# Kernel optimization log

Measured on AMD Instinct MI355X. Metric: run time of the kernel, lower is better.

The kernel has to match this reference:

```python
import jax, jax.numpy as jnp
import numpy as np

# Dims (match init_kwargs)
B, S, D = 2, 2048, 2048
H = 16
Q_LORA, KV_LORA = 768, 512
NOPE, ROPE, VD = 128, 64, 128
QHD = NOPE + ROPE  # 192


def setup_inputs() -> dict:
    key = jax.random.key(0)
    ks = jax.random.split(key, 7)
    w = lambda k, shape: (jax.random.normal(k, shape, jnp.float32) * 0.02)
    return {
        "x": jax.random.normal(ks[0], (B, S, D), jnp.float32),
        "position": jnp.broadcast_to(jnp.arange(S, dtype=jnp.int32), (B, S)),
        "mask": jnp.tril(jnp.ones((1, 1, S, S), jnp.int32)),  # causal
        "w_q_down": w(ks[1], (D, Q_LORA)),                 # (in, out) layout
        "w_q_up": w(ks[2], (Q_LORA, H * QHD)),
        "w_kv_down": w(ks[3], (D, KV_LORA + ROPE)),
        "w_kv_up": w(ks[4], (KV_LORA, H * (NOPE + VD))),
        "w_out": w(ks[5], (H * VD, D)),
    }


def reference(x, position, mask, w_q_down, w_q_up, w_kv_down, w_kv_up, w_out):
    # position unused: rope_embedding is None in the source module.
    # Low-rank Q: down then up projection.
    q = (x @ w_q_down) @ w_q_up                      # [B,S,H*QHD]
    q = q.reshape(B, S, H, QHD).transpose(0, 2, 1, 3)  # [B,H,S,QHD]
    q_nope, q_rope = q[..., :NOPE], q[..., NOPE:]

    # Low-rank KV: down projection yields compressed kv + shared rope key.
    c = x @ w_kv_down                                # [B,S,KV_LORA+ROPE]
    c_kv, k_rope = c[..., :KV_LORA], c[..., KV_LORA:]
    k_rope = k_rope[:, None, :, :]                   # [B,1,S,ROPE]

    kv = (c_kv @ w_kv_up).reshape(B, S, H, NOPE + VD).transpose(0, 2, 1, 3)
    k_nope, v = kv[..., :NOPE], kv[..., NOPE:]       # [B,H,S,NOPE], [B,H,S,VD]

    q_state = jnp.concatenate([q_nope, q_rope], axis=-1)           # [B,H,S,QHD]
    k_state = jnp.concatenate(
        [k_nope, jnp.broadcast_to(k_rope, (B, H, S, ROPE))], axis=-1)

    scale = 1.0 / jnp.sqrt(jnp.float32(VD))  # source divides by sqrt(v_head_dim)
    scores = jnp.einsum("bhqd,bhkd->bhqk", q_state, k_state) * scale
    scores = jnp.where(mask == 0, jnp.float32(-jnp.inf), scores)
    att = jax.nn.softmax(scores, axis=-1)            # dropout_rate=0 (eval)
    out = jnp.einsum("bhqk,bhkd->bhqd", att, v)      # [B,H,S,VD]
    out = out.transpose(0, 2, 1, 3).reshape(B, S, H * VD)
    return out @ w_out
```

## Files before the change

### kernel.cpp

```cpp
#include <hip/hip_runtime.h>

typedef __bf16 bf16;
typedef bf16 bf16x8 __attribute__((ext_vector_type(8)));
typedef bf16 bf16x4 __attribute__((ext_vector_type(4)));
typedef float f32x4 __attribute__((ext_vector_type(4)));
typedef short s16x4 __attribute__((ext_vector_type(4)));

#define AS1 __attribute__((address_space(1)))
#define AS3 __attribute__((address_space(3)))

__device__ __forceinline__ void load_lds16(const void* g, void* l) {
    __builtin_amdgcn_global_load_lds((const AS1 unsigned int*)g,
                                     (AS3 unsigned int*)l, 16, 0, 0);
}

__global__ __launch_bounds__(256) void cast_f32_bf16(
        const float* __restrict__ in, bf16* __restrict__ out, int n) {
    int i = (blockIdx.x * 256 + threadIdx.x) * 4;
    if (i < n) {
        float4 v = *(const float4*)(in + i);
        bf16x4 o = { (bf16)v.x, (bf16)v.y, (bf16)v.z, (bf16)v.w };
        *(bf16x4*)(out + i) = o;
    }
}

__global__ __launch_bounds__(256) void transpose_cast(
        const float* __restrict__ in, bf16* __restrict__ out,
        int K, int N, int Np) {
    __shared__ float tile[32][33];
    int bx = blockIdx.x * 32;
    int by = blockIdx.y * 32;
    int tx = threadIdx.x, ty = threadIdx.y;
#pragma unroll
    for (int i = 0; i < 4; ++i) {
        int k = by + ty + i * 8, n = bx + tx;
        float v = (k < K && n < N) ? in[(size_t)k * N + n] : 0.f;
        tile[ty + i * 8][tx] = v;
    }
    __syncthreads();
#pragma unroll
    for (int i = 0; i < 4; ++i) {
        int n = bx + ty + i * 8, k = by + tx;
        if (n < Np && k < K) out[(size_t)n * K + k] = (bf16)tile[tx][ty + i * 8];
    }
}

__global__ __launch_bounds__(256) void transpose_v(
        const bf16* __restrict__ kvb, bf16* __restrict__ vtb) {
    __shared__ bf16 t[32][34];
    const int kv0 = blockIdx.x * 32;
    const int vd0 = blockIdx.y * 32;
    const int bh = blockIdx.z;
    const int b = bh >> 4, h = bh & 15;
    const int tx = threadIdx.x, ty = threadIdx.y;
#pragma unroll
    for (int i = 0; i < 4; ++i)
        t[ty + i * 8][tx] = kvb[(size_t)(b * 2048 + kv0 + ty + i * 8) * 4096
                                + h * 256 + 128 + vd0 + tx];
    __syncthreads();
#pragma unroll
    for (int i = 0; i < 4; ++i)
        vtb[(size_t)(bh * 128 + vd0 + ty + i * 8) * 2048 + kv0 + tx] =
            t[tx][ty + i * 8];
}

template <typename OutT>
__global__ __launch_bounds__(256) void gemm_bt(
        const bf16* __restrict__ A, const bf16* __restrict__ Bt,
        OutT* __restrict__ C, int K, int lda, int ldb, int ldc) {
    __shared__ __align__(16) bf16 As[128 * 64];
    __shared__ __align__(16) bf16 Bs[128 * 64];
    const int tid = threadIdx.x;
    const int wave = tid >> 6, lane = tid & 63;
    const int l15 = lane & 15, quad = lane >> 4;
    const int m0 = blockIdx.y * 128, n0 = blockIdx.x * 128;
    const int wm = (wave >> 1) * 64, wn = (wave & 1) * 64;

    f32x4 acc[4][4] = {};

    for (int k0 = 0; k0 < K; k0 += 64) {
#pragma unroll
        for (int c = 0; c < 4; ++c) {
            int e = wave * 2048 + c * 512 + lane * 8;
            int r = e >> 6, col = e & 63;
            load_lds16(A + (size_t)(m0 + r) * lda + k0 + col,
                       &As[wave * 2048 + c * 512]);
            load_lds16(Bt + (size_t)(n0 + r) * ldb + k0 + col,
                       &Bs[wave * 2048 + c * 512]);
        }
        __syncthreads();
#pragma unroll
        for (int kk = 0; kk < 64; kk += 32) {
            bf16x8 af[4], bf[4];
#pragma unroll
            for (int i = 0; i < 4; ++i)
                af[i] = *(const bf16x8*)&As[(wm + i * 16 + l15) * 64 + kk + quad * 8];
#pragma unroll
            for (int j = 0; j < 4; ++j)
                bf[j] = *(const bf16x8*)&Bs[(wn + j * 16 + l15) * 64 + kk + quad * 8];
#pragma unroll
            for (int i = 0; i < 4; ++i)
#pragma unroll
                for (int j = 0; j < 4; ++j)
                    acc[i][j] = __builtin_amdgcn_mfma_f32_16x16x32_bf16(
                        af[i], bf[j], acc[i][j], 0, 0, 0);
        }
        __syncthreads();
    }
#pragma unroll
    for (int i = 0; i < 4; ++i)
#pragma unroll
        for (int j = 0; j < 4; ++j) {
            int row = m0 + wm + i * 16 + quad * 4;
            int col = n0 + wn + j * 16 + l15;
#pragma unroll
            for (int r = 0; r < 4; ++r)
                C[(size_t)(row + r) * ldc + col] = (OutT)acc[i][j][r];
        }
}

__global__ __launch_bounds__(256) void gemm_down(
        const bf16* __restrict__ A, const bf16* __restrict__ Bt,
        bf16* __restrict__ C1, bf16* __restrict__ C2) {
    const int K = 2048, lda = 2048, ldb = 2048;
    __shared__ __align__(16) bf16 As[128 * 64];
    __shared__ __align__(16) bf16 Bs[128 * 64];
    const int tid = threadIdx.x;
    const int wave = tid >> 6, lane = tid & 63;
    const int l15 = lane & 15, quad = lane >> 4;
    const int m0 = blockIdx.y * 128, n0 = blockIdx.x * 128;
    const int wm = (wave >> 1) * 64, wn = (wave & 1) * 64;

    f32x4 acc[4][4] = {};

    for (int k0 = 0; k0 < K; k0 += 64) {
#pragma unroll
        for (int c = 0; c < 4; ++c) {
            int e = wave * 2048 + c * 512 + lane * 8;
            int r = e >> 6, col = e & 63;
            load_lds16(A + (size_t)(m0 + r) * lda + k0 + col,
                       &As[wave * 2048 + c * 512]);
            load_lds16(Bt + (size_t)(n0 + r) * ldb + k0 + col,
                       &Bs[wave * 2048 + c * 512]);
        }
        __syncthreads();
#pragma unroll
        for (int kk = 0; kk < 64; kk += 32) {
            bf16x8 af[4], bf[4];
#pragma unroll
            for (int i = 0; i < 4; ++i)
                af[i] = *(const bf16x8*)&As[(wm + i * 16 + l15) * 64 + kk + quad * 8];
#pragma unroll
            for (int j = 0; j < 4; ++j)
                bf[j] = *(const bf16x8*)&Bs[(wn + j * 16 + l15) * 64 + kk + quad * 8];
#pragma unroll
            for (int i = 0; i < 4; ++i)
#pragma unroll
                for (int j = 0; j < 4; ++j)
                    acc[i][j] = __builtin_amdgcn_mfma_f32_16x16x32_bf16(
                        af[i], bf[j], acc[i][j], 0, 0, 0);
        }
        __syncthreads();
    }
    bf16* Cp; int ldc, coff;
    if (n0 < 768) { Cp = C1; ldc = 768; coff = 0; }
    else          { Cp = C2; ldc = 640; coff = 768; }
#pragma unroll
    for (int i = 0; i < 4; ++i)
#pragma unroll
        for (int j = 0; j < 4; ++j) {
            int row = m0 + wm + i * 16 + quad * 4;
            int col = n0 + wn + j * 16 + l15 - coff;
#pragma unroll
            for (int r = 0; r < 4; ++r)
                Cp[(size_t)(row + r) * ldc + col] = (bf16)acc[i][j][r];
        }
}

__global__ __launch_bounds__(256) void mla_attention_split(
        const bf16* __restrict__ qb, const bf16* __restrict__ kvb,
        const bf16* __restrict__ cb, const bf16* __restrict__ vtb,
        bf16* __restrict__ ob, bf16* __restrict__ part_o,
        float* __restrict__ part_ml) {
    constexpr int S = 2048;
    const int idx = 47 - blockIdx.x;
    const int h = blockIdx.y, b = blockIdx.z;
    int qt, t0, t1, c;
    if (idx < 16) { qt = idx; t0 = 0; t1 = qt + 1; c = -1; }
    else {
        qt = 16 + ((idx - 16) >> 1);
        c = (idx - 16) & 1;
        if (c == 0) { t0 = 0;  t1 = 16; }
        else        { t0 = 16; t1 = qt + 1; }
    }
    const int q0 = qt * 64;
    const int tid = threadIdx.x, wave = tid >> 6, lane = tid & 63;
    const int l15 = lane & 15, quad = lane >> 4;

    __shared__ __align__(16) bf16 Ks[2][24 * 512];
    __shared__ __align__(16) bf16 Vs[2][8 * 1024];

    const int qrow = q0 + wave * 16 + l15;
    bf16x8 qf[6];
    {
        const bf16* qr = qb + (size_t)(b * S + qrow) * 3072 + h * 192;
#pragma unroll
        for (int ks = 0; ks < 6; ++ks)
            qf[ks] = *(const bf16x8*)(qr + ks * 32 + quad * 8);
    }

    const bf16* vt_head = vtb + (size_t)((b * 16 + h) * 128) * 2048;

    auto stage = [&](int kt, int bufi) {
        const int kv0 = kt * 64;
#pragma unroll
        for (int i = 0; i < 6; ++i) {
            const size_t row = (size_t)(b * S + kv0 + wave * 16 + l15);
            const bf16* g = (i < 4)
                ? kvb + row * 4096 + h * 256 + i * 32 + quad * 8
                : cb  + row * 640  + 512 + (i - 4) * 32 + quad * 8;
            load_lds16(g, &Ks[bufi][(wave * 6 + i) * 512]);
        }
#pragma unroll
        for (int j = 0; j < 2; ++j)
#pragma unroll
            for (int i = 0; i < 2; ++i) {
                const bf16* g = vt_head
                    + (size_t)((wave * 2 + j) * 16 + l15) * 2048
                    + kv0 + (i * 4 + quad) * 8;
                load_lds16(g, &Vs[bufi][(wave * 2 + j) * 1024 + i * 512]);
            }
    };

    f32x4 o[8] = {};
    float m_i = -1e30f, l_i = 0.f;
    const float sm_scale = 0.08838834764831845f * 1.4426950408889634f;
    const int qmin_w = q0 + wave * 16;

    stage(t0, 0);
    if (t0 + 1 < t1) stage(t0 + 1, 1);

    int cur = 0;
    for (int kt = t0; kt < t1; ++kt, cur ^= 1) {
        const int kv0 = kt * 64;

        if (kt + 1 < t1) asm volatile("s_waitcnt vmcnt(10)" ::: "memory");
        else             asm volatile("s_waitcnt vmcnt(0)" ::: "memory");
        __builtin_amdgcn_s_barrier();
        __builtin_amdgcn_sched_barrier(0);

        f32x4 s[4];
        __builtin_amdgcn_s_setprio(1);
#pragma unroll
        for (int mt = 0; mt < 4; ++mt) {
            f32x4 a = {};
#pragma unroll
            for (int ks = 0; ks < 6; ++ks) {
                bf16x8 kf = *(const bf16x8*)&Ks[cur][(mt * 6 + ks) * 512 + lane * 8];
                a = __builtin_amdgcn_mfma_f32_16x16x32_bf16(kf, qf[ks], a, 0, 0, 0);
            }
            s[mt] = a;
        }
        __builtin_amdgcn_s_setprio(0);

        float mx = -1e30f;
        if (kv0 + 63 > qmin_w) {
#pragma unroll
            for (int mt = 0; mt < 4; ++mt)
#pragma unroll
                for (int r = 0; r < 4; ++r) {
                    int kvi = kv0 + mt * 16 + quad * 4 + r;
                    float v = (kvi <= qrow) ? s[mt][r] * sm_scale : -1e30f;
                    s[mt][r] = v;
                    mx = fmaxf(mx, v);
                }
        } else {
#pragma unroll
            for (int mt = 0; mt < 4; ++mt)
#pragma unroll
                for (int r = 0; r < 4; ++r) {
                    float v = s[mt][r] * sm_scale;
                    s[mt][r] = v;
                    mx = fmaxf(mx, v);
                }
        }
        mx = fmaxf(mx, __shfl_xor(mx, 16, 64));
        mx = fmaxf(mx, __shfl_xor(mx, 32, 64));
        float m_new = fmaxf(m_i, mx);
        float su = 0.f;
        bf16x4 pf[4];
#pragma unroll
        for (int mt = 0; mt < 4; ++mt)
#pragma unroll
            for (int r = 0; r < 4; ++r) {
                float pv = exp2f(s[mt][r] - m_new);
                su += pv;
                pf[mt][r] = (bf16)pv;
            }
        su += __shfl_xor(su, 16, 64);
        su += __shfl_xor(su, 32, 64);
        float alpha = exp2f(m_i - m_new);
        l_i = l_i * alpha + su;
        m_i = m_new;
        float alpha_r[4];
#pragma unroll
        for (int r = 0; r < 4; ++r) alpha_r[r] = __shfl(alpha, quad * 4 + r, 64);
#pragma unroll
        for (int nt = 0; nt < 8; ++nt)
#pragma unroll
            for (int r = 0; r < 4; ++r) o[nt][r] *= alpha_r[r];

        __builtin_amdgcn_s_setprio(1);
#pragma unroll
        for (int ktk = 0; ktk < 4; ++ktk) {
            s16x4 a = __builtin_bit_cast(s16x4, pf[ktk]);
            const int voff = ktk * 256 + (quad >> 1) * 128 + l15 * 8 + (quad & 1) * 4;
#pragma unroll
            for (int nt = 0; nt < 8; ++nt) {
                s16x4 bfv = __builtin_bit_cast(s16x4,
                    *(const bf16x4*)&Vs[cur][nt * 1024 + voff]);
                o[nt] = __builtin_amdgcn_mfma_f32_16x16x16bf16_1k(a, bfv, o[nt], 0, 0, 0);
            }
        }
        __builtin_amdgcn_s_setprio(0);

        __builtin_amdgcn_s_barrier();
        if (kt + 2 < t1) stage(kt + 2, cur);
    }

    if (c < 0) {
        float l_r[4];
#pragma unroll
        for (int r = 0; r < 4; ++r) l_r[r] = __shfl(l_i, quad * 4 + r, 64);
        bf16* obase = ob + (size_t)(b * S + q0 + wave * 16) * 2048 + h * 128;
#pragma unroll
        for (int nt = 0; nt < 8; ++nt)
#pragma unroll
            for (int r = 0; r < 4; ++r)
                obase[(size_t)(quad * 4 + r) * 2048 + nt * 16 + l15] =
                    (bf16)(o[nt][r] / l_r[r]);
    } else {
        const int slot0 = (b * 16 + h) * 16 + (qt - 16);
        if (quad == 0) {
            const int qlocal = wave * 16 + l15;
            part_ml[(slot0 * 2 + c) * 128 + qlocal] = m_i;
            part_ml[(slot0 * 2 + c) * 128 + 64 + qlocal] = l_i;
        }
        if (c == 0) {
            bf16* pb = part_o + (size_t)slot0 * 8192
                       + (size_t)(wave * 16) * 128;
#pragma unroll
            for (int nt = 0; nt < 8; ++nt)
#pragma unroll
                for (int r = 0; r < 4; ++r)
                    pb[(quad * 4 + r) * 128 + nt * 16 + l15] = (bf16)o[nt][r];
        } else {
            bf16* obase = ob + (size_t)(b * S + q0 + wave * 16) * 2048 + h * 128;
#pragma unroll
            for (int nt = 0; nt < 8; ++nt)
#pragma unroll
                for (int r = 0; r < 4; ++r)
                    obase[(size_t)(quad * 4 + r) * 2048 + nt * 16 + l15] =
                        (bf16)o[nt][r];
        }
    }
}

__global__ __launch_bounds__(256) void mla_merge(
        const bf16* __restrict__ part_o, const float* __restrict__ part_ml,
        bf16* __restrict__ ob) {
    const int qt = 16 + blockIdx.x, h = blockIdx.y, b = blockIdx.z;
    const int slot0 = (b * 16 + h) * 16 + (qt - 16);
    const int tid = threadIdx.x;
    const int row = tid >> 2;
    const int col = (tid & 3) * 32;
    const float* ml0 = part_ml + (size_t)(slot0 * 2) * 128;
    const float* ml1 = ml0 + 128;
    const float m0 = ml0[row], l0v = ml0[64 + row];
    const float m1 = ml1[row], l1v = ml1[64 + row];
    const float M = fmaxf(m0, m1);
    float a0 = exp2f(m0 - M), a1 = exp2f(m1 - M);
    const float inv = 1.f / (l0v * a0 + l1v * a1);
    a0 *= inv; a1 *= inv;
    const bf16* p0 = part_o + (size_t)slot0 * 8192 + row * 128 + col;
    bf16* po = ob + (size_t)(b * 2048 + qt * 64 + row) * 2048 + h * 128 + col;
#pragma unroll
    for (int i = 0; i < 4; ++i) {
        bf16x8 v0 = *(const bf16x8*)(p0 + i * 8);
        bf16x8 v1 = *(const bf16x8*)(po + i * 8);
        bf16x8 om;
#pragma unroll
        for (int u = 0; u < 8; ++u)
            om[u] = (bf16)((float)v0[u] * a0 + (float)v1[u] * a1);
        *(bf16x8*)(po + i * 8) = om;
    }
}

extern "C" void kernel_launch(void* const* d_in, const int* in_sizes, int n_in,
                              void* d_out, int out_size, void* d_ws, size_t ws_size,
                              hipStream_t stream) {
    const float* x    = (const float*)d_in[0];
    const float* wqd  = (const float*)d_in[3];
    const float* wqu  = (const float*)d_in[4];
    const float* wkvd = (const float*)d_in[5];
    const float* wkvu = (const float*)d_in[6];
    const float* wout = (const float*)d_in[7];
    float* out = (float*)d_out;
    char* ws = (char*)d_ws;

    bf16* xb    = (bf16*)(ws + 0);
    bf16* vtb   = (bf16*)(ws + 0);
    bf16* wqdT  = (bf16*)(ws + 16777216);
    bf16* wkvdT = (bf16*)(ws + 19922944);
    bf16* wquT  = (bf16*)(ws + 22544384);
    bf16* wkvuT = (bf16*)(ws + 27262976);
    bf16* part_o  = (bf16*)(ws + 16777216);
    float* part_ml = (float*)(ws + 25165824);
    bf16* woutT = (bf16*)(ws + 31457280);
    bf16* qd    = (bf16*)(ws + 39845888);
    bf16* qb    = (bf16*)(ws + 46137344);
    bf16* cb    = (bf16*)(ws + 71303168);
    bf16* kvb   = (bf16*)(ws + 76546048);
    bf16* attnb = (bf16*)(ws + 110100480);

    dim3 tb(32, 8);
    cast_f32_bf16<<<8192, 256, 0, stream>>>(x, xb, 8388608);
    transpose_cast<<<dim3(24, 64),  tb, 0, stream>>>(wqd,  wqdT,  2048, 768,  768);
    transpose_cast<<<dim3(20, 64),  tb, 0, stream>>>(wkvd, wkvdT, 2048, 576,  640);
    transpose_cast<<<dim3(96, 24),  tb, 0, stream>>>(wqu,  wquT,  768,  3072, 3072);
    transpose_cast<<<dim3(128, 16), tb, 0, stream>>>(wkvu, wkvuT, 512,  4096, 4096);
    transpose_cast<<<dim3(64, 64),  tb, 0, stream>>>(wout, woutT, 2048, 2048, 2048);

    gemm_down<<<dim3(11, 32), 256, 0, stream>>>(xb, wqdT, qd, cb);
    gemm_bt<bf16><<<dim3(24, 32), 256, 0, stream>>>(qd, wquT,  qb,  768, 768, 768, 3072);
    gemm_bt<bf16><<<dim3(32, 32), 256, 0, stream>>>(cb, wkvuT, kvb, 512, 640, 512, 4096);

    transpose_v<<<dim3(64, 4, 32), tb, 0, stream>>>(kvb, vtb);

    mla_attention_split<<<dim3(48, 16, 2), 256, 0, stream>>>(
        qb, kvb, cb, vtb, attnb, part_o, part_ml);
    mla_merge<<<dim3(16, 16, 2), 256, 0, stream>>>(part_o, part_ml, attnb);

    gemm_bt<float><<<dim3(16, 32), 256, 0, stream>>>(attnb, woutT, out, 2048, 2048, 2048, 2048);
}
```

Baseline: 490.4 us.

## Widen attention blocks to 128 query rows with 8 waves sharing K/V tiles

The attention kernel now runs 512-thread blocks covering 128 query rows. The 8 waves split the K/V staging work, so each staged 64-key tile is reused by twice as many query rows and global-to-LDS traffic per query drops. The split/merge bookkeeping is rescaled to 128-row tiles. The softmax reductions become tree-shaped, and the rescale of the output accumulators is skipped when no row's max increased. The cost is half as many blocks, plus a coarser causal split that can leave per-block work less balanced.

```diff
diff --git a/kernel.cpp b/kernel.cpp
--- a/kernel.cpp
+++ b/kernel.cpp
@@ -177,23 +177,23 @@
         }
 }
 
-__global__ __launch_bounds__(256) void mla_attention_split(
+__global__ __launch_bounds__(512, 4) void mla_attention_split(
         const bf16* __restrict__ qb, const bf16* __restrict__ kvb,
         const bf16* __restrict__ cb, const bf16* __restrict__ vtb,
         bf16* __restrict__ ob, bf16* __restrict__ part_o,
         float* __restrict__ part_ml) {
     constexpr int S = 2048;
-    const int idx = 47 - blockIdx.x;
+    const int idx = 23 - blockIdx.x;
     const int h = blockIdx.y, b = blockIdx.z;
     int qt, t0, t1, c;
-    if (idx < 16) { qt = idx; t0 = 0; t1 = qt + 1; c = -1; }
+    if (idx < 8) { qt = idx; t0 = 0; t1 = 2 * qt + 2; c = -1; }
     else {
-        qt = 16 + ((idx - 16) >> 1);
-        c = (idx - 16) & 1;
+        qt = 8 + ((idx - 8) >> 1);
+        c = (idx - 8) & 1;
         if (c == 0) { t0 = 0;  t1 = 16; }
-        else        { t0 = 16; t1 = qt + 1; }
-    }
-    const int q0 = qt * 64;
+        else        { t0 = 16; t1 = 2 * qt + 2; }
+    }
+    const int q0 = qt * 128;
     const int tid = threadIdx.x, wave = tid >> 6, lane = tid & 63;
     const int l15 = lane & 15, quad = lane >> 4;
 
@@ -213,23 +213,22 @@
 
     auto stage = [&](int kt, int bufi) {
         const int kv0 = kt * 64;
-#pragma unroll
-        for (int i = 0; i < 6; ++i) {
-            const size_t row = (size_t)(b * S + kv0 + wave * 16 + l15);
-            const bf16* g = (i < 4)
-                ? kvb + row * 4096 + h * 256 + i * 32 + quad * 8
-                : cb  + row * 640  + 512 + (i - 4) * 32 + quad * 8;
-            load_lds16(g, &Ks[bufi][(wave * 6 + i) * 512]);
-        }
-#pragma unroll
-        for (int j = 0; j < 2; ++j)
-#pragma unroll
-            for (int i = 0; i < 2; ++i) {
-                const bf16* g = vt_head
-                    + (size_t)((wave * 2 + j) * 16 + l15) * 2048
-                    + kv0 + (i * 4 + quad) * 8;
-                load_lds16(g, &Vs[bufi][(wave * 2 + j) * 1024 + i * 512]);
-            }
+        const int mt = wave >> 1;
+        const size_t row = (size_t)(b * S + kv0 + mt * 16 + l15);
+#pragma unroll
+        for (int i = 0; i < 3; ++i) {
+            const int ks = (wave & 1) * 3 + i;
+            const bf16* g = (ks < 4)
+                ? kvb + row * 4096 + h * 256 + ks * 32 + quad * 8
+                : cb  + row * 640  + 512 + (ks - 4) * 32 + quad * 8;
+            load_lds16(g, &Ks[bufi][(mt * 6 + ks) * 512]);
+        }
+#pragma unroll
+        for (int i = 0; i < 2; ++i) {
+            const bf16* g = vt_head + (size_t)(wave * 16 + l15) * 2048
+                            + kv0 + (i * 4 + quad) * 8;
+            load_lds16(g, &Vs[bufi][wave * 1024 + i * 512]);
+        }
     };
 
     f32x4 o[8] = {};
@@ -238,13 +237,13 @@
     const int qmin_w = q0 + wave * 16;
 
     stage(t0, 0);
-    if (t0 + 1 < t1) stage(t0 + 1, 1);
+    stage(t0 + 1, 1);
 
     int cur = 0;
     for (int kt = t0; kt < t1; ++kt, cur ^= 1) {
         const int kv0 = kt * 64;
 
-        if (kt + 1 < t1) asm volatile("s_waitcnt vmcnt(10)" ::: "memory");
+        if (kt + 1 < t1) asm volatile("s_waitcnt vmcnt(5)" ::: "memory");
         else             asm volatile("s_waitcnt vmcnt(0)" ::: "memory");
         __builtin_amdgcn_s_barrier();
         __builtin_amdgcn_sched_barrier(0);
@@ -263,52 +262,60 @@
         }
         __builtin_amdgcn_s_setprio(0);
 
-        float mx = -1e30f;
         if (kv0 + 63 > qmin_w) {
 #pragma unroll
             for (int mt = 0; mt < 4; ++mt)
 #pragma unroll
                 for (int r = 0; r < 4; ++r) {
                     int kvi = kv0 + mt * 16 + quad * 4 + r;
-                    float v = (kvi <= qrow) ? s[mt][r] * sm_scale : -1e30f;
-                    s[mt][r] = v;
-                    mx = fmaxf(mx, v);
+                    s[mt][r] = (kvi <= qrow) ? s[mt][r] * sm_scale : -1e30f;
                 }
         } else {
 #pragma unroll
             for (int mt = 0; mt < 4; ++mt)
 #pragma unroll
-                for (int r = 0; r < 4; ++r) {
-                    float v = s[mt][r] * sm_scale;
-                    s[mt][r] = v;
-                    mx = fmaxf(mx, v);
-                }
-        }
+                for (int r = 0; r < 4; ++r)
+                    s[mt][r] = s[mt][r] * sm_scale;
+        }
+        float mx4[4];
+#pragma unroll
+        for (int mt = 0; mt < 4; ++mt)
+            mx4[mt] = fmaxf(fmaxf(s[mt][0], s[mt][1]),
+                            fmaxf(s[mt][2], s[mt][3]));
+        float mx = fmaxf(fmaxf(mx4[0], mx4[1]), fmaxf(mx4[2], mx4[3]));
         mx = fmaxf(mx, __shfl_xor(mx, 16, 64));
         mx = fmaxf(mx, __shfl_xor(mx, 32, 64));
         float m_new = fmaxf(m_i, mx);
-        float su = 0.f;
+        float su4[4];
         bf16x4 pf[4];
 #pragma unroll
-        for (int mt = 0; mt < 4; ++mt)
-#pragma unroll
-            for (int r = 0; r < 4; ++r) {
-                float pv = exp2f(s[mt][r] - m_new);
-                su += pv;
-                pf[mt][r] = (bf16)pv;
-            }
+        for (int mt = 0; mt < 4; ++mt) {
+            float e0 = exp2f(s[mt][0] - m_new);
+            float e1 = exp2f(s[mt][1] - m_new);
+            float e2 = exp2f(s[mt][2] - m_new);
+            float e3 = exp2f(s[mt][3] - m_new);
+            su4[mt] = (e0 + e1) + (e2 + e3);
+            pf[mt][0] = (bf16)e0; pf[mt][1] = (bf16)e1;
+            pf[mt][2] = (bf16)e2; pf[mt][3] = (bf16)e3;
+        }
+        float su = (su4[0] + su4[1]) + (su4[2] + su4[3]);
         su += __shfl_xor(su, 16, 64);
         su += __shfl_xor(su, 32, 64);
-        float alpha = exp2f(m_i - m_new);
-        l_i = l_i * alpha + su;
-        m_i = m_new;
-        float alpha_r[4];
-#pragma unroll
-        for (int r = 0; r < 4; ++r) alpha_r[r] = __shfl(alpha, quad * 4 + r, 64);
-#pragma unroll
-        for (int nt = 0; nt < 8; ++nt)
-#pragma unroll
-            for (int r = 0; r < 4; ++r) o[nt][r] *= alpha_r[r];
+        if (__all(mx <= m_i)) {
+            l_i += su;
+        } else {
+            float alpha = exp2f(m_i - m_new);
+            l_i = l_i * alpha + su;
+            m_i = m_new;
+            float alpha_r[4];
+#pragma unroll
+            for (int r = 0; r < 4; ++r)
+                alpha_r[r] = __shfl(alpha, quad * 4 + r, 64);
+#pragma unroll
+            for (int nt = 0; nt < 8; ++nt)
+#pragma unroll
+                for (int r = 0; r < 4; ++r) o[nt][r] *= alpha_r[r];
+        }
 
         __builtin_amdgcn_s_setprio(1);
 #pragma unroll
@@ -340,14 +347,14 @@
                 obase[(size_t)(quad * 4 + r) * 2048 + nt * 16 + l15] =
                     (bf16)(o[nt][r] / l_r[r]);
     } else {
-        const int slot0 = (b * 16 + h) * 16 + (qt - 16);
+        const int slot = (b * 16 + h) * 8 + (qt - 8);
         if (quad == 0) {
             const int qlocal = wave * 16 + l15;
-            part_ml[(slot0 * 2 + c) * 128 + qlocal] = m_i;
-            part_ml[(slot0 * 2 + c) * 128 + 64 + qlocal] = l_i;
+            part_ml[(slot * 2 + c) * 256 + qlocal] = m_i;
+            part_ml[(slot * 2 + c) * 256 + 128 + qlocal] = l_i;
         }
         if (c == 0) {
-            bf16* pb = part_o + (size_t)slot0 * 8192
+            bf16* pb = part_o + (size_t)slot * 16384
                        + (size_t)(wave * 16) * 128;
 #pragma unroll
             for (int nt = 0; nt < 8; ++nt)
@@ -369,23 +376,23 @@
 __global__ __launch_bounds__(256) void mla_merge(
         const bf16* __restrict__ part_o, const float* __restrict__ part_ml,
         bf16* __restrict__ ob) {
-    const int qt = 16 + blockIdx.x, h = blockIdx.y, b = blockIdx.z;
-    const int slot0 = (b * 16 + h) * 16 + (qt - 16);
+    const int qt = 8 + blockIdx.x, h = blockIdx.y, b = blockIdx.z;
+    const int slot = (b * 16 + h) * 8 + (qt - 8);
     const int tid = threadIdx.x;
-    const int row = tid >> 2;
-    const int col = (tid & 3) * 32;
-    const float* ml0 = part_ml + (size_t)(slot0 * 2) * 128;
-    const float* ml1 = ml0 + 128;
-    const float m0 = ml0[row], l0v = ml0[64 + row];
-    const float m1 = ml1[row], l1v = ml1[64 + row];
+    const int row = tid >> 1;
+    const int col = (tid & 1) * 64;
+    const float* ml0 = part_ml + (size_t)(slot * 2) * 256;
+    const float* ml1 = ml0 + 256;
+    const float m0 = ml0[row], l0v = ml0[128 + row];
+    const float m1 = ml1[row], l1v = ml1[128 + row];
     const float M = fmaxf(m0, m1);
     float a0 = exp2f(m0 - M), a1 = exp2f(m1 - M);
     const float inv = 1.f / (l0v * a0 + l1v * a1);
     a0 *= inv; a1 *= inv;
-    const bf16* p0 = part_o + (size_t)slot0 * 8192 + row * 128 + col;
-    bf16* po = ob + (size_t)(b * 2048 + qt * 64 + row) * 2048 + h * 128 + col;
-#pragma unroll
-    for (int i = 0; i < 4; ++i) {
+    const bf16* p0 = part_o + (size_t)slot * 16384 + row * 128 + col;
+    bf16* po = ob + (size_t)(b * 2048 + qt * 128 + row) * 2048 + h * 128 + col;
+#pragma unroll
+    for (int i = 0; i < 8; ++i) {
         bf16x8 v0 = *(const bf16x8*)(p0 + i * 8);
         bf16x8 v1 = *(const bf16x8*)(po + i * 8);
         bf16x8 om;
@@ -437,9 +444,9 @@
 
     transpose_v<<<dim3(64, 4, 32), tb, 0, stream>>>(kvb, vtb);
 
-    mla_attention_split<<<dim3(48, 16, 2), 256, 0, stream>>>(
+    mla_attention_split<<<dim3(24, 16, 2), 512, 0, stream>>>(
         qb, kvb, cb, vtb, attnb, part_o, part_ml);
-    mla_merge<<<dim3(16, 16, 2), 256, 0, stream>>>(part_o, part_ml, attnb);
+    mla_merge<<<dim3(8, 16, 2), 256, 0, stream>>>(part_o, part_ml, attnb);
 
     gemm_bt<float><<<dim3(16, 32), 256, 0, stream>>>(attnb, woutT, out, 2048, 2048, 2048, 2048);
 }
```

New measurement: 472.0 us. -3.7%, faster.
